# Performance work log

Hardware: AMD Instinct MI355X
Metric: run time of the kernel (lower is better)

The kernel has to match this reference:

```python
import jax, jax.numpy as jnp
import numpy as np
import math

LOG2PI = math.log(2.0 * math.pi)


def _pair_sum(m1, v1, m2, v2, w):
    """sum_{i,j} w[i,j] * exp(delta_ij) for diagonal 2-D Gaussians.

    m1,v1: [K1,2] means / diagonal variances; m2,v2: [K2,2]; w: [K1,K2].
    Closed form of the torch code's 2x2 inverse/det/mm chain exploiting the
    fact that all covariances are diagonal (cov = diag((wh/2)^2)).
    """
    ci = 1.0 / v1[:, None, :]                      # [K1,1,2] = cov_inv_i diag
    cj = 1.0 / v2[None, :, :]                      # [1,K2,2] = cov_inv_j diag
    s = ci + cj                                    # [K1,K2,2] = cov_inv_ij diag
    mij = (m1[:, None, :] * ci + m2[None, :, :] * cj) / s   # combined mean
    quad = (jnp.sum(mij * mij * s, -1)
            - jnp.sum(m1 * m1 / v1, -1)[:, None]
            - jnp.sum(m2 * m2 / v2, -1)[None, :])            # [K1,K2]
    # log(det(cov_inv_ij) / (det(cov_inv_i) * det(cov_inv_j)))
    logdet = (jnp.sum(jnp.log(s), -1)
              + jnp.sum(jnp.log(v1), -1)[:, None]
              + jnp.sum(jnp.log(v2), -1)[None, :])           # [K1,K2]
    delta = 0.5 * (quad - logdet - 2.0 * LOG2PI)   # x_dim = 2
    return jnp.sum(w * jnp.exp(delta))


def _cs_div(p_m, p_v, p_a, q_m, q_v, q_a):
    pq = _pair_sum(p_m, p_v, q_m, q_v, p_a @ q_a.T)
    pp = _pair_sum(p_m, p_v, p_m, p_v, p_a @ p_a.T)
    qq = _pair_sum(q_m, q_v, q_m, q_v, q_a @ q_a.T)
    return 2.0 * jnp.log(pq) - jnp.log(pp) - jnp.log(qq)


def _forward(pred_bboxes, pred_labels, gt_bboxes, gt_labels):
    num_classes = pred_labels.shape[2] - 1
    pred_alpha = (jax.nn.sigmoid(pred_labels[:, :, -1])[:, :, None]
                  * jax.nn.softmax(pred_labels[:, :, :-1], axis=2))   # [bs,kp,C]
    gt_alpha = jax.nn.one_hot(gt_labels, num_classes, dtype=pred_alpha.dtype)
    pred_m = pred_bboxes[:, :, :2]
    pred_v = jnp.square(pred_bboxes[:, :, 2:] / 2.0)
    gt_m = gt_bboxes[:, :, :2]
    gt_v = jnp.square(gt_bboxes[:, :, 2:] / 2.0)
    per_img = jax.vmap(_cs_div)(gt_m, gt_v, gt_alpha, pred_m, pred_v, pred_alpha)
    return -jnp.sum(per_img)


def setup_inputs() -> dict:
    key = jax.random.key(0)
    k1, k2, k3, k4 = jax.random.split(key, 4)
    BS, KP, KG, NC = 32, 1000, 100, 80
    # widths/heights must be strictly positive -> uniform in [0.05, 1)
    pred_bboxes = jax.random.uniform(k1, (BS, KP, 4), jnp.float32, 0.05, 1.0)
    pred_labels = jax.random.normal(k2, (BS, KP, NC + 1), jnp.float32)
    gt_bboxes = jax.random.uniform(k3, (BS, KG, 4), jnp.float32, 0.05, 1.0)
    gt_labels = jax.random.randint(k4, (BS, KG), 0, NC)
    return {"pred_bboxes": pred_bboxes, "pred_labels": pred_labels,
            "gt_bboxes": gt_bboxes, "gt_labels": gt_labels}


def reference(pred_bboxes, pred_labels, gt_bboxes, gt_labels):
    return _forward(pred_bboxes, pred_labels, gt_bboxes, gt_labels)
```

## Files before the change

kernel.cpp:

```cpp
#include <hip/hip_runtime.h>
#include <math.h>

#define BS 32
#define KP 1000
#define KPP 1024
#define KG 100
#define NC 80
#define SK 96
#define LP 104
#define NT 8
#define NIT 15
#define NQQ (BS * NIT)
#define NPPQ (5 * BS)
#define NALL (NQQ + NPPQ)
#define NPERIMG 20
#define GCNT 512

using bf16x8 = __attribute__((ext_vector_type(8))) short;
using f32x4  = __attribute__((ext_vector_type(4))) float;
using f32x2  = __attribute__((ext_vector_type(2))) float;

__device__ __forceinline__ float wave_reduce_sum(float v) {
#pragma unroll
    for (int m = 32; m > 0; m >>= 1) v += __shfl_xor(v, m, 64);
    return v;
}
__device__ __forceinline__ float wave_reduce_max(float v) {
#pragma unroll
    for (int m = 32; m > 0; m >>= 1) v = fmaxf(v, __shfl_xor(v, m, 64));
    return v;
}

__device__ __forceinline__ unsigned short f2bf(float f) {
    unsigned int u = __float_as_uint(f);
    u += 0x7fffu + ((u >> 16) & 1u);
    return (unsigned short)(u >> 16);
}
__device__ __forceinline__ float bf2f(unsigned short h) {
    return __uint_as_float(((unsigned int)h) << 16);
}

__device__ __forceinline__ float kval(float4 a, float4 b) {
    f32x2 S = (f32x2){a.z, a.w} + (f32x2){b.z, b.w};
    f32x2 d = (f32x2){a.x, a.y} - (f32x2){b.x, b.y};
    f32x2 d2 = d * d;
    f32x2 t = d2 * S.yx;
    float num = t.x + t.y;
    float P = S.x * S.y;
    float rs = __builtin_amdgcn_rsqf(P);
    float q = num * rs * rs;
    return 0.15915494309189535f * rs * __expf(-0.5f * q);
}

__global__ __launch_bounds__(256) void alpha_kernel(const float* __restrict__ pl,
                                                    unsigned short* __restrict__ ah,
                                                    float* __restrict__ acc) {
    if (blockIdx.x == 0) {
#pragma unroll
        for (int k = 0; k < 3; ++k) acc[threadIdx.x + 256 * k] = 0.0f;
    }
    int wave = threadIdx.x >> 6;
    int lane = threadIdx.x & 63;
    int rr = blockIdx.x * 4 + wave;
    int b = rr >> 10, r = rr & (KPP - 1);
    unsigned short* oh = ah + (size_t)rr * SK;
    if (r < KP) {
        const float* x = pl + ((size_t)b * KP + r) * (NC + 1);
        float l0 = x[lane];
        float l1 = (lane < 16) ? x[64 + lane] : -1e30f;
        float obj = x[NC];
        float m = wave_reduce_max(fmaxf(l0, l1));
        float e0 = __expf(l0 - m);
        float e1 = (lane < 16) ? __expf(l1 - m) : 0.0f;
        float s = wave_reduce_sum(e0 + e1);
        float sig = 1.0f / (1.0f + __expf(-obj));
        float sc = sig / s;
        oh[lane] = f2bf(e0 * sc);
        if (lane < 32) oh[64 + lane] = (lane < 16) ? f2bf(e1 * sc) : 0;
    } else {
        oh[lane] = 0;
        if (lane < 32) oh[64 + lane] = 0;
    }
}

__global__ __launch_bounds__(256, 3) void main_kernel(const float* __restrict__ pb,
                                                      const unsigned short* __restrict__ ahg,
                                                      const float* __restrict__ gtb,
                                                      const int* __restrict__ gtl,
                                                      float* __restrict__ acc,
                                                      float* __restrict__ out) {
    __shared__ short lds[2 * 128 * LP];
    __shared__ float red[4];
    __shared__ int last;

    int tid = threadIdx.x;
    int lane = tid & 63, w = tid >> 6;
    int bi = blockIdx.x;
    int b;

    if (bi < NQQ) {
        short* la = lds;
        short* lb = lds + 128 * LP;
        b = bi & 31;
        int p = bi >> 5;
        int it = p >> 1, half = p & 1;
        int i0 = it * 128;

        if (tid < 128) {
            int gi = i0 + tid;
            float4 v = make_float4(0.0f, 0.0f, 1.0f, 1.0f);
            if (gi < KP) {
                float4 x = ((const float4*)pb)[b * KP + gi];
                v = make_float4(x.x, x.y, 0.25f * x.z * x.z, 0.25f * x.w * x.w);
            }
            *(float4*)(la + tid * LP + 96) = v;
        }
        {
            const float4* sa = (const float4*)(ahg + ((size_t)(b << 10) + i0) * SK);
#pragma unroll
            for (int k = 0; k < 6; ++k) {
                int o = tid + k * 256;
                int row = o / 12, slot = o - row * 12;
                *(float4*)(la + row * LP + slot * 8) = sa[o];
            }
        }

        int wy = w >> 1, wx = w & 1;
        int m15 = lane & 15, quad = lane >> 4;
        int ar = wy * 64 + m15;
        int br = wx * 64 + m15;
        int jb = wx * 64 + m15;
        int ib = wy * 64 + quad * 4;

        float part = 0.0f;
        bool first = true;
        for (int jt = it + half; jt < NT; jt += 2) {
            int j0 = jt * 128;
            if (!first) __syncthreads();
            if (tid < 128) {
                int gi = j0 + tid;
                float4 v = make_float4(0.0f, 0.0f, 1.0f, 1.0f);
                if (gi < KP) {
                    float4 x = ((const float4*)pb)[b * KP + gi];
                    v = make_float4(x.x, x.y, 0.25f * x.z * x.z, 0.25f * x.w * x.w);
                }
                *(float4*)(lb + tid * LP + 96) = v;
            }
            {
                const float4* sb = (const float4*)(ahg + ((size_t)(b << 10) + j0) * SK);
#pragma unroll
                for (int k = 0; k < 6; ++k) {
                    int o = tid + k * 256;
                    int row = o / 12, slot = o - row * 12;
                    *(float4*)(lb + row * LP + slot * 8) = sb[o];
                }
            }
            __syncthreads();

            f32x4 c4[4][4];
#pragma unroll
            for (int r = 0; r < 4; ++r)
#pragma unroll
                for (int s = 0; s < 4; ++s) c4[r][s] = (f32x4){0.0f, 0.0f, 0.0f, 0.0f};

#pragma unroll
            for (int ks = 0; ks < 3; ++ks) {
                int kk = ks * 32 + quad * 8;
                bf16x8 bh[4];
#pragma unroll
                for (int cg = 0; cg < 4; ++cg)
                    bh[cg] = *(const bf16x8*)(lb + (br + cg * 16) * LP + kk);
#pragma unroll
                for (int rg = 0; rg < 4; ++rg) {
                    bf16x8 xh = *(const bf16x8*)(la + (ar + rg * 16) * LP + kk);
#pragma unroll
                    for (int cg = 0; cg < 4; ++cg)
                        c4[rg][cg] = __builtin_amdgcn_mfma_f32_16x16x32_bf16(xh, bh[cg], c4[rg][cg], 0, 0, 0);
                }
            }

            float4 pj[4];
#pragma unroll
            for (int cg = 0; cg < 4; ++cg)
                pj[cg] = *(const float4*)(lb + (jb + cg * 16) * LP + 96);
            float tpart = 0.0f;
#pragma unroll
            for (int rg = 0; rg < 4; ++rg) {
#pragma unroll
                for (int e = 0; e < 4; ++e) {
                    float4 pi = *(const float4*)(la + (ib + rg * 16 + e) * LP + 96);
#pragma unroll
                    for (int cg = 0; cg < 4; ++cg)
                        tpart += c4[rg][cg][e] * kval(pi, pj[cg]);
                }
            }
            part += (jt != it) ? 2.0f * tpart : tpart;
            first = false;
        }

        part = wave_reduce_sum(part);
        if (lane == 0) red[w] = part;
        __syncthreads();
        if (tid == 0)
            atomicAdd(&acc[b * 16 + 2], red[0] + red[1] + red[2] + red[3]);
    } else {
        int pi = bi - NQQ;
        b = pi & 31;
        int p5 = pi >> 5;
        short* lalpha = lds;
        float4* gm = (float4*)(lds + 24576);
        int* gl = (int*)(lds + 24576 + 800);
        if (tid < KG) {
            float4 x = ((const float4*)gtb)[b * KG + tid];
            gm[tid] = make_float4(x.x, x.y, 0.25f * x.z * x.z, 0.25f * x.w * x.w);
            gl[tid] = gtl[b * KG + tid];
        }
        if (p5 < 4) {
            const float4* sa = (const float4*)(ahg + ((size_t)(b << 10) + p5 * 256) * SK);
#pragma unroll
            for (int k = 0; k < 12; ++k) {
                int o = tid + k * 256;
                *(float4*)(lalpha + o * 8) = sa[o];
            }
        }
        __syncthreads();
        float part = 0.0f;
        if (p5 < 4) {
            int j = p5 * 256 + tid;
            if (j < KP) {
                float4 x = ((const float4*)pb)[b * KP + j];
                float4 pm = make_float4(x.x, x.y, 0.25f * x.z * x.z, 0.25f * x.w * x.w);
                const unsigned short* arow = (const unsigned short*)lalpha + tid * SK;
#pragma unroll 4
                for (int i = 0; i < KG; ++i) {
                    part += bf2f(arow[gl[i]]) * kval(gm[i], pm);
                }
            }
        } else {
            for (int p = tid; p < KG * KG; p += 256) {
                int i = p / KG;
                int j = p - i * KG;
                if (gl[i] == gl[j]) part += kval(gm[i], gm[j]);
            }
        }
        part = wave_reduce_sum(part);
        if (lane == 0) red[w] = part;
        __syncthreads();
        if (tid == 0) {
            float s = red[0] + red[1] + red[2] + red[3];
            atomicAdd(&acc[b * 16 + ((p5 < 4) ? 0 : 1)], s);
        }
    }

    if (tid == 0) {
        __threadfence();
        unsigned int o = atomicAdd((unsigned int*)(acc + b * 16 + 4), 1u);
        int l = 0;
        if (o == NPERIMG - 1) {
            __threadfence();
            unsigned int g = atomicAdd((unsigned int*)(acc + GCNT), 1u);
            l = (g == BS - 1) ? 1 : 0;
        }
        last = l;
    }
    __syncthreads();
    if (last && tid < 64) {
        float v = 0.0f;
        if (tid < BS) {
            float pq = atomicAdd(&acc[tid * 16 + 0], 0.0f);
            float pp = atomicAdd(&acc[tid * 16 + 1], 0.0f);
            float qq = atomicAdd(&acc[tid * 16 + 2], 0.0f);
            v = 2.0f * logf(pq) - logf(pp) - logf(qq);
        }
        v = wave_reduce_sum(v);
        if (tid == 0) out[0] = -v;
    }
}

extern "C" void kernel_launch(void* const* d_in, const int* in_sizes, int n_in,
                              void* d_out, int out_size, void* d_ws, size_t ws_size,
                              hipStream_t stream) {
    (void)in_sizes; (void)n_in; (void)out_size; (void)ws_size;
    const float* pred_bb  = (const float*)d_in[0];
    const float* pred_lab = (const float*)d_in[1];
    const float* gt_bb    = (const float*)d_in[2];
    const int*   gt_lab   = (const int*)d_in[3];
    float* out = (float*)d_out;

    unsigned short* ah = (unsigned short*)d_ws;
    float* acc = (float*)(ah + (size_t)BS * KPP * SK);

    hipLaunchKernelGGL(alpha_kernel, dim3(BS * KPP / 4), dim3(256), 0, stream,
                       pred_lab, ah, acc);
    hipLaunchKernelGGL(main_kernel, dim3(NALL), dim3(256), 0, stream,
                       pred_bb, ah, gt_bb, gt_lab, acc, out);
}
```

Before: 99.25 us.

## Prefetch next B tile into registers to overlap global loads with MFMA

Next j-tile's alpha rows and box params are loaded into registers before compute on the current tile, then written to LDS at the top of the next iteration, so global latency hides behind the MFMA and kernel math. kval is rewritten with scalar fmaf instead of 2-wide vectors, and the accumulation uses fmaf. This raises register pressure (six float4 plus one float4 per thread), which could lower occupancy.

New measurement: 163.3 us. 64.6% more time.

```diff
diff --git a/kernel.cpp b/kernel.cpp
--- a/kernel.cpp
+++ b/kernel.cpp
@@ -18,7 +18,6 @@
 
 using bf16x8 = __attribute__((ext_vector_type(8))) short;
 using f32x4  = __attribute__((ext_vector_type(4))) float;
-using f32x2  = __attribute__((ext_vector_type(2))) float;
 
 __device__ __forceinline__ float wave_reduce_sum(float v) {
 #pragma unroll
@@ -41,13 +40,11 @@
 }
 
 __device__ __forceinline__ float kval(float4 a, float4 b) {
-    f32x2 S = (f32x2){a.z, a.w} + (f32x2){b.z, b.w};
-    f32x2 d = (f32x2){a.x, a.y} - (f32x2){b.x, b.y};
-    f32x2 d2 = d * d;
-    f32x2 t = d2 * S.yx;
-    float num = t.x + t.y;
-    float P = S.x * S.y;
+    float Sx = a.z + b.z, Sy = a.w + b.w;
+    float dx = a.x - b.x, dy = a.y - b.y;
+    float P  = Sx * Sy;
     float rs = __builtin_amdgcn_rsqf(P);
+    float num = fmaf(dx * dx, Sy, dy * dy * Sx);
     float q = num * rs * rs;
     return 0.15915494309189535f * rs * __expf(-0.5f * q);
 }
@@ -106,17 +103,20 @@
         int it = p >> 1, half = p & 1;
         int i0 = it * 128;
 
+        const float4* pbb = (const float4*)pb + (size_t)b * KP;
+        const unsigned short* ahb = ahg + ((size_t)b << 10) * SK;
+
         if (tid < 128) {
             int gi = i0 + tid;
             float4 v = make_float4(0.0f, 0.0f, 1.0f, 1.0f);
             if (gi < KP) {
-                float4 x = ((const float4*)pb)[b * KP + gi];
+                float4 x = pbb[gi];
                 v = make_float4(x.x, x.y, 0.25f * x.z * x.z, 0.25f * x.w * x.w);
             }
             *(float4*)(la + tid * LP + 96) = v;
         }
         {
-            const float4* sa = (const float4*)(ahg + ((size_t)(b << 10) + i0) * SK);
+            const float4* sa = (const float4*)(ahb + (size_t)i0 * SK);
 #pragma unroll
             for (int k = 0; k < 6; ++k) {
                 int o = tid + k * 256;
@@ -131,28 +131,49 @@
         int br = wx * 64 + m15;
         int jb = wx * 64 + m15;
         int ib = wy * 64 + quad * 4;
+        int rowq = tid / 12, slotq = tid - rowq * 12;
+
+        int jt = it + half;
+        float4 a_pre[6];
+        float4 p_pre = make_float4(0.0f, 0.0f, 2.0f, 2.0f);
+        {
+            const float4* sb = (const float4*)(ahb + (size_t)(jt * 128) * SK);
+#pragma unroll
+            for (int k = 0; k < 6; ++k) a_pre[k] = sb[tid + k * 256];
+            if (tid < 128) {
+                int gi = jt * 128 + tid;
+                if (gi < KP) p_pre = pbb[gi];
+                else p_pre = make_float4(0.0f, 0.0f, 2.0f, 2.0f);
+            }
+        }
 
         float part = 0.0f;
         bool first = true;
-        for (int jt = it + half; jt < NT; jt += 2) {
-            int j0 = jt * 128;
+        while (jt < NT) {
             if (!first) __syncthreads();
             if (tid < 128) {
-                int gi = j0 + tid;
-                float4 v = make_float4(0.0f, 0.0f, 1.0f, 1.0f);
-                if (gi < KP) {
-                    float4 x = ((const float4*)pb)[b * KP + gi];
-                    v = make_float4(x.x, x.y, 0.25f * x.z * x.z, 0.25f * x.w * x.w);
-                }
+                float4 v = make_float4(p_pre.x, p_pre.y,
+                                       0.25f * p_pre.z * p_pre.z,
+                                       0.25f * p_pre.w * p_pre.w);
                 *(float4*)(lb + tid * LP + 96) = v;
             }
-            {
-                const float4* sb = (const float4*)(ahg + ((size_t)(b << 10) + j0) * SK);
-#pragma unroll
-                for (int k = 0; k < 6; ++k) {
-                    int o = tid + k * 256;
-                    int row = o / 12, slot = o - row * 12;
-                    *(float4*)(lb + row * LP + slot * 8) = sb[o];
+#pragma unroll
+            for (int k = 0; k < 6; ++k) {
+                int o = tid + k * 256;
+                int row = (k == 0) ? rowq : o / 12;
+                int slot = (k == 0) ? slotq : o - row * 12;
+                *(float4*)(lb + row * LP + slot * 8) = a_pre[k];
+            }
+            int jcur = jt;
+            jt += 2;
+            if (jt < NT) {
+                const float4* sb = (const float4*)(ahb + (size_t)(jt * 128) * SK);
+#pragma unroll
+                for (int k = 0; k < 6; ++k) a_pre[k] = sb[tid + k * 256];
+                if (tid < 128) {
+                    int gi = jt * 128 + tid;
+                    if (gi < KP) p_pre = pbb[gi];
+                    else p_pre = make_float4(0.0f, 0.0f, 2.0f, 2.0f);
                 }
             }
             __syncthreads();
@@ -191,10 +212,10 @@
                     float4 pi = *(const float4*)(la + (ib + rg * 16 + e) * LP + 96);
 #pragma unroll
                     for (int cg = 0; cg < 4; ++cg)
-                        tpart += c4[rg][cg][e] * kval(pi, pj[cg]);
+                        tpart = fmaf(c4[rg][cg][e], kval(pi, pj[cg]), tpart);
                 }
             }
-            part += (jt != it) ? 2.0f * tpart : tpart;
+            part += (jcur != it) ? 2.0f * tpart : tpart;
             first = false;
         }
 
```
